# Kernel tuning notes

Measured on AMD Instinct MI355X. Metric: run time of the kernel, lower is better.

The kernel has to match this reference:

```python
import jax, jax.numpy as jnp
import numpy as np
from jax import lax

N_FT = 1024          # Fourier grid size (module default n_ft)
X_RANGE = 0.3        # module default x_range: data rescaled into torus
TWO_PI = 2.0 * np.pi


def gaussian_sliced_kernel_ft(h, d, sigma_sq):
    """Fourier coefficients of the 1D basis function whose slicing gives the
    d-dim Gaussian kernel exp(-r^2/(2 sigma^2)):
        khat(h) = (2 pi^2 sigma^2)^(d/2) |h|^(d-1) exp(-2 pi^2 sigma^2 h^2) / Gamma(d/2)
    Computed in log-space for numerical stability (|h|^(d-1) overflows for d=64).
    """
    habs = jnp.abs(h)
    logv = (0.5 * d) * jnp.log(2.0 * np.pi ** 2 * sigma_sq) \
        + (d - 1.0) * jnp.log(jnp.where(habs > 0, habs, 1.0)) \
        - 2.0 * np.pi ** 2 * sigma_sq * h ** 2 \
        - lax.lgamma(jnp.asarray(d / 2.0, dtype=jnp.float32))
    return jnp.where(habs > 0, jnp.exp(logv), 0.0).astype(jnp.float32)


def setup_inputs():
    key = jax.random.key(0)
    k1, k2, k3, k4 = jax.random.split(key, 4)
    N, M, d, P = 8192, 8192, 64, 64
    x = jax.random.normal(k1, (N, d), dtype=jnp.float32)
    y = jax.random.normal(k2, (M, d), dtype=jnp.float32)
    x_weights = jax.random.normal(k3, (N,), dtype=jnp.float32)
    xis = jax.random.normal(k4, (P, d), dtype=jnp.float32)
    xis = xis / jnp.linalg.norm(xis, axis=-1, keepdims=True)  # unit slice directions
    scale = jnp.ones((1,), dtype=jnp.float32)
    return {"x": x, "y": y, "x_weights": x_weights, "scale": scale, "xis": xis}


def reference(x, y, x_weights, scale, xis):
    # Sliced fast Gaussian kernel summation:
    #   out(y_m) = (1/P) sum_p sum_n w_n k1d(<xi_p, x_n - y_m>)
    # where the 1D convolution per slice is evaluated through its Fourier series
    # (the exact NDFT sum that the module's NFFT approximates).
    d = x.shape[1]
    scale_s = jnp.reshape(scale, ())
    # precomputation: rescale data so all points fit in the torus window
    norm_max = jnp.maximum(jnp.max(jnp.linalg.norm(x, axis=-1)),
                           jnp.max(jnp.linalg.norm(y, axis=-1)))
    sf = X_RANGE / norm_max
    xs, ys = x * sf, y * sf
    scale_r = scale_s * sf
    h = jnp.arange(-(N_FT // 2), N_FT // 2, dtype=jnp.float32)  # (K,) frequencies
    kft = gaussian_sliced_kernel_ft(h, d, scale_r ** 2)          # (K,) real, symmetric
    w = x_weights.astype(jnp.complex64)

    def one_slice(acc, xi):
        a = xs @ xi  # (N,) projected source points
        b = ys @ xi  # (M,) projected target points
        # adjoint NDFT: yhat_k = sum_n w_n exp(2 pi i h_k a_n)
        yhat = jnp.exp(1j * TWO_PI * h[:, None] * a[None, :]) @ w        # (K,)
        # forward NDFT at targets: s_m = sum_k kft_k * yhat_k * exp(-2 pi i h_k b_m)
        s = jnp.exp(-1j * TWO_PI * b[:, None] * h[None, :]) @ (kft * yhat)  # (M,)
        return acc + s.real.astype(jnp.float32), None

    acc0 = jnp.zeros(y.shape[0], dtype=jnp.float32)
    total, _ = lax.scan(one_slice, acc0, xis)  # sequential over slices = batch_size_P
    return total / xis.shape[0]
```

## Files before the change

### kernel.cpp

```cpp
#include <hip/hip_runtime.h>
#include <math.h>

#define N_SRC 8192
#define D_DIM 64
#define P_SL  64
#define KH    512

#define WS_NM    0
#define WS_CS    16
#define WS_A     (WS_CS + P_SL*KH*2)
#define WS_B2    (WS_A + P_SL*N_SRC)

#define LOG_THRESH (-23.0259f)
#define LGAMMA32    78.0922236f
#define TWO_PI2     19.7392088f

__device__ __forceinline__ void sincos2pi(float t, float& s, float& c) {
    float f = __builtin_amdgcn_fractf(t);
    s = __builtin_amdgcn_sinf(f);
    c = __builtin_amdgcn_cosf(f);
}

__global__ __launch_bounds__(256) void kA(const float* __restrict__ x,
                                          const float* __restrict__ y,
                                          const float* __restrict__ xis,
                                          float* __restrict__ ws,
                                          float* __restrict__ out) {
    int tid = threadIdx.x, b = blockIdx.x;
    int rblk = b & 63, q = b >> 6;
    int r = rblk * 256 + tid;
    int isx = (r < N_SRC);
    const float* src = isx ? (x + (size_t)r * D_DIM)
                           : (y + (size_t)(r - N_SRC) * D_DIM);
    float4 row[16];
    const float4* rp = (const float4*)src;
#pragma unroll
    for (int j = 0; j < 16; ++j) row[j] = rp[j];

    if (q == 0) {
        float ss = 0.f;
#pragma unroll
        for (int j = 0; j < 16; ++j) {
            ss = fmaf(row[j].x, row[j].x, ss); ss = fmaf(row[j].y, row[j].y, ss);
            ss = fmaf(row[j].z, row[j].z, ss); ss = fmaf(row[j].w, row[j].w, ss);
        }
        float nm = sqrtf(ss);
        for (int o = 32; o; o >>= 1) nm = fmaxf(nm, __shfl_xor(nm, o, 64));
        if ((tid & 63) == 0)
            atomicMax((int*)ws + WS_NM, __float_as_int(nm));
    }

    int gtid = b * 256 + tid;
    if (gtid < P_SL * KH * 2) ws[WS_CS + gtid] = 0.f;
    if (gtid < N_SRC)         out[gtid] = 0.f;

    int rr = isx ? r : r - N_SRC;
    float* dst = ws + (isx ? WS_A : WS_B2);
    for (int pi = 0; pi < 8; ++pi) {
        int p = q * 8 + pi;
        const float4* xi = (const float4*)(xis + p * D_DIM);
        float acc = 0.f;
#pragma unroll
        for (int j = 0; j < 16; ++j) {
            float4 u = xi[j];
            acc = fmaf(row[j].x, u.x, acc); acc = fmaf(row[j].y, u.y, acc);
            acc = fmaf(row[j].z, u.z, acc); acc = fmaf(row[j].w, u.w, acc);
        }
        dst[(size_t)p * N_SRC + rr] = acc;
    }
}

__global__ __launch_bounds__(256) void kB(const float* __restrict__ xw,
                                          const float* __restrict__ scale,
                                          float* __restrict__ ws) {
    __shared__ int skmin, skmax;
    __shared__ float sC[64], sS[64];
    int tid = threadIdx.x;
    int chunk = blockIdx.x, p = blockIdx.y;
    if (tid == 0) { skmin = 0x7fffffff; skmax = 0; }
    __syncthreads();
    float nm = __int_as_float(((const int*)ws)[WS_NM]);
    float sf = 0.3f / nm;
    float sr = scale[0] * sf;
    float a = TWO_PI2 * sr * sr;
    float la = logf(a);
    for (int k = tid + 1; k <= KH; k += 256) {
        float logv = 32.f * la + 63.f * logf((float)k)
                   - a * (float)k * (float)k - LGAMMA32;
        if (logv > LOG_THRESH) { atomicMin(&skmin, k); atomicMax(&skmax, k); }
    }
    __syncthreads();
    int kmin = skmin, kmax = skmax;
    if (kmax == 0) return;
    int kcnt = kmax - kmin + 1;
    int lane = tid & 63;

    int base = chunk * 1024 + tid;
    const float* ap = ws + WS_A + (size_t)p * N_SRC;
    float pa_[4], pw_[4], th_[4], rc_[4], rs_[4];
#pragma unroll
    for (int j = 0; j < 4; ++j) {
        pa_[j] = ap[base + 256 * j];
        pw_[j] = xw[base + 256 * j];
        th_[j] = pa_[j] * sf;
        sincos2pi(th_[j], rs_[j], rc_[j]);
    }

    for (int kbase = 0; kbase < kcnt; kbase += 64) {
        __syncthreads();
        if (tid < 64) { sC[tid] = 0.f; sS[tid] = 0.f; }
        __syncthreads();

        float accC[64], accS[64];
        float pc_[4], ps_[4];
#pragma unroll
        for (int blk = 0; blk < 4; ++blk) {
            float f0 = (float)(kmin + kbase + blk * 16);
#pragma unroll
            for (int j = 0; j < 4; ++j) {
                float t0 = th_[j] * f0;
                float ss0, cc0; sincos2pi(t0, ss0, cc0);
                pc_[j] = cc0 * pw_[j];
                ps_[j] = ss0 * pw_[j];
            }
#pragma unroll
            for (int u = 0; u < 16; ++u) {
                int i = blk * 16 + u;
                accC[i] = (pc_[0] + pc_[1]) + (pc_[2] + pc_[3]);
                accS[i] = (ps_[0] + ps_[1]) + (ps_[2] + ps_[3]);
#pragma unroll
                for (int j = 0; j < 4; ++j) {
                    float nc = fmaf(pc_[j], rc_[j], -(ps_[j] * rs_[j]));
                    float ns = fmaf(ps_[j], rc_[j],  pc_[j] * rs_[j]);
                    pc_[j] = nc; ps_[j] = ns;
                }
            }
        }

#pragma unroll
        for (int h = 32; h >= 1; h >>= 1) {
            bool hb = (lane & h) != 0;
#pragma unroll
            for (int i = 0; i < h; ++i) {
                float sc = hb ? accC[i]     : accC[i + h];
                float ssv = hb ? accS[i]     : accS[i + h];
                float kc = hb ? accC[i + h] : accC[i];
                float ks = hb ? accS[i + h] : accS[i];
                accC[i] = kc + __shfl_xor(sc, h, 64);
                accS[i] = ks + __shfl_xor(ssv, h, 64);
            }
        }
        atomicAdd(&sC[lane], accC[0]);
        atomicAdd(&sS[lane], accS[0]);
        __syncthreads();

        int ki = kbase + tid;
        if (tid < 64 && ki < kcnt) {
            int kk = kmin + ki;
            float logv = 32.f * la + 63.f * logf((float)kk)
                       - a * (float)kk * (float)kk - LGAMMA32;
            float wk = ((kk == KH) ? 1.f : 2.f) * expf(logv) * (1.f / (float)P_SL);
            atomicAdd(ws + WS_CS + ((size_t)p * KH + ki) * 2 + 0, wk * sC[tid]);
            atomicAdd(ws + WS_CS + ((size_t)p * KH + ki) * 2 + 1, wk * sS[tid]);
        }
    }
}

__global__ __launch_bounds__(256) void kC(const float* __restrict__ scale,
                                          float* __restrict__ ws,
                                          float* __restrict__ out) {
    __shared__ int skmin, skmax;
    int tid = threadIdx.x;
    if (tid == 0) { skmin = 0x7fffffff; skmax = 0; }
    __syncthreads();
    float nm = __int_as_float(((const int*)ws)[WS_NM]);
    float sf = 0.3f / nm;
    float sr = scale[0] * sf;
    float a = TWO_PI2 * sr * sr;
    float la = logf(a);
    for (int k = tid + 1; k <= KH; k += 256) {
        float logv = 32.f * la + 63.f * logf((float)k)
                   - a * (float)k * (float)k - LGAMMA32;
        if (logv > LOG_THRESH) { atomicMin(&skmin, k); atomicMax(&skmax, k); }
    }
    __syncthreads();
    int kmin = skmin, kmax = skmax;
    if (kmax == 0) return;
    int kcnt = kmax - kmin + 1;
    int m = blockIdx.x * 256 + tid;
    int pg = blockIdx.y;
    float sum = 0.f;
    for (int pi = 0; pi < 4; ++pi) {
        int p = pg * 4 + pi;
        float bm = ws[WS_B2 + (size_t)p * N_SRC + m] * sf;
        const float2* cs = (const float2*)(ws + WS_CS) + (size_t)p * KH;
        float cr, crs; sincos2pi(bm, crs, cr);
        for (int ib = 0; ib < kcnt; ib += 8) {
            float t0 = bm * (float)(kmin + ib);
            float c, s; sincos2pi(t0, s, c);
#pragma unroll
            for (int u = 0; u < 8; ++u) {
                int i = ib + u;
                if (i < kcnt) {
                    float2 q = cs[i];
                    sum = fmaf(q.x, c, sum);
                    sum = fmaf(q.y, s, sum);
                }
                float nc = fmaf(c, cr, -(s * crs));
                s = fmaf(s, cr, c * crs);
                c = nc;
            }
        }
    }
    atomicAdd(out + m, sum);
}

extern "C" void kernel_launch(void* const* d_in, const int* in_sizes, int n_in,
                              void* d_out, int out_size, void* d_ws, size_t ws_size,
                              hipStream_t stream) {
    const float* x     = (const float*)d_in[0];
    const float* y     = (const float*)d_in[1];
    const float* xw    = (const float*)d_in[2];
    const float* scale = (const float*)d_in[3];
    const float* xis   = (const float*)d_in[4];
    float* ws  = (float*)d_ws;
    float* out = (float*)d_out;

    kA<<<dim3(512),      dim3(256), 0, stream>>>(x, y, xis, ws, out);
    kB<<<dim3(8, 64),    dim3(256), 0, stream>>>(xw, scale, ws);
    kC<<<dim3(32, 16),   dim3(256), 0, stream>>>(scale, ws, out);
}
```

Baseline: 108.2 us.

## Have each projection block compute 32 slices with four concurrent dot products

The projection kernel now launches 128 blocks instead of 512. Each block handles 32 slice directions per row rather than 8, so each x/y row is loaded from global memory once per 32 projections instead of once per 8. The inner loop computes four slice dot products at a time with independent accumulators to expose more instruction-level parallelism. The zero-initialisation of the coefficient buffer becomes a strided loop to keep full coverage with fewer threads. The trade-off is fewer blocks than compute units on a large GPU and more register pressure per thread.

```diff
diff --git a/kernel.cpp b/kernel.cpp
--- a/kernel.cpp
+++ b/kernel.cpp
@@ -51,22 +51,35 @@
     }
 
     int gtid = b * 256 + tid;
-    if (gtid < P_SL * KH * 2) ws[WS_CS + gtid] = 0.f;
-    if (gtid < N_SRC)         out[gtid] = 0.f;
+    for (int z = gtid; z < P_SL * KH * 2; z += 128 * 256)
+        ws[WS_CS + z] = 0.f;
+    if (gtid < N_SRC) out[gtid] = 0.f;
 
     int rr = isx ? r : r - N_SRC;
     float* dst = ws + (isx ? WS_A : WS_B2);
-    for (int pi = 0; pi < 8; ++pi) {
-        int p = q * 8 + pi;
-        const float4* xi = (const float4*)(xis + p * D_DIM);
-        float acc = 0.f;
+    for (int pi = 0; pi < 32; pi += 4) {
+        int p0 = q * 32 + pi;
+        const float4* xi0 = (const float4*)(xis + (p0 + 0) * D_DIM);
+        const float4* xi1 = (const float4*)(xis + (p0 + 1) * D_DIM);
+        const float4* xi2 = (const float4*)(xis + (p0 + 2) * D_DIM);
+        const float4* xi3 = (const float4*)(xis + (p0 + 3) * D_DIM);
+        float a0 = 0.f, a1 = 0.f, a2 = 0.f, a3 = 0.f;
 #pragma unroll
         for (int j = 0; j < 16; ++j) {
-            float4 u = xi[j];
-            acc = fmaf(row[j].x, u.x, acc); acc = fmaf(row[j].y, u.y, acc);
-            acc = fmaf(row[j].z, u.z, acc); acc = fmaf(row[j].w, u.w, acc);
-        }
-        dst[(size_t)p * N_SRC + rr] = acc;
+            float4 u0 = xi0[j], u1 = xi1[j], u2 = xi2[j], u3 = xi3[j];
+            a0 = fmaf(row[j].x, u0.x, a0); a0 = fmaf(row[j].y, u0.y, a0);
+            a0 = fmaf(row[j].z, u0.z, a0); a0 = fmaf(row[j].w, u0.w, a0);
+            a1 = fmaf(row[j].x, u1.x, a1); a1 = fmaf(row[j].y, u1.y, a1);
+            a1 = fmaf(row[j].z, u1.z, a1); a1 = fmaf(row[j].w, u1.w, a1);
+            a2 = fmaf(row[j].x, u2.x, a2); a2 = fmaf(row[j].y, u2.y, a2);
+            a2 = fmaf(row[j].z, u2.z, a2); a2 = fmaf(row[j].w, u2.w, a2);
+            a3 = fmaf(row[j].x, u3.x, a3); a3 = fmaf(row[j].y, u3.y, a3);
+            a3 = fmaf(row[j].z, u3.z, a3); a3 = fmaf(row[j].w, u3.w, a3);
+        }
+        dst[(size_t)(p0 + 0) * N_SRC + rr] = a0;
+        dst[(size_t)(p0 + 1) * N_SRC + rr] = a1;
+        dst[(size_t)(p0 + 2) * N_SRC + rr] = a2;
+        dst[(size_t)(p0 + 3) * N_SRC + rr] = a3;
     }
 }
 
@@ -226,7 +239,7 @@
     float* ws  = (float*)d_ws;
     float* out = (float*)d_out;
 
-    kA<<<dim3(512),      dim3(256), 0, stream>>>(x, y, xis, ws, out);
+    kA<<<dim3(128),      dim3(256), 0, stream>>>(x, y, xis, ws, out);
     kB<<<dim3(8, 64),    dim3(256), 0, stream>>>(xw, scale, ws);
     kC<<<dim3(32, 16),   dim3(256), 0, stream>>>(scale, ws, out);
 }
```

Measured after the change: 117.8 us. +8.9%, slower.
